# Performance work log

Hardware: AMD Instinct MI355X
Metric: run time of the kernel (lower is better)

## Reference

```python
import math
import jax, jax.numpy as jnp
import numpy as np

B, N, D, H, NI, NL, NS, MID = 32, 2048, 256, 8, 64, 3, 32, 3


def _ln(x, g, b, eps=1e-5):
    m = jnp.mean(x, axis=-1, keepdims=True)
    v = jnp.mean((x - m) ** 2, axis=-1, keepdims=True)
    return (x - m) * jax.lax.rsqrt(v + eps) * g + b


def _mab(Q, K, mask, Wq, bq, Wk, bk, Wv, bv, Wo, bo, g0, b0, g1, b1):
    # torch's split(dim_split,2)+cat(...,0) == reshape to (B, n, H, dh)
    dh = D // H
    q = (Q @ Wq + bq).reshape(Q.shape[0], Q.shape[1], H, dh)
    k = (K @ Wk + bk).reshape(K.shape[0], K.shape[1], H, dh)
    v = (K @ Wv + bv).reshape(K.shape[0], K.shape[1], H, dh)
    A = jnp.einsum('bqhd,bkhd->bhqk', q, k) / math.sqrt(D)  # note: sqrt(dim_V), faithful
    A = jnp.where(mask[:, None, None, :] == 0, -1e4, A)
    A = jax.nn.softmax(A, axis=-1)
    o = q + jnp.einsum('bhqk,bkhd->bqhd', A, v)
    O = o.reshape(Q.shape[0], Q.shape[1], D)
    O = _ln(O, g0, b0)
    O = O + jax.nn.relu(O @ Wo + bo)
    return _ln(O, g1, b1)


def _forward(x_values, y_target, point_mask, proj_W, proj_b, isab_I,
             isab_Wq, isab_bq, isab_Wk, isab_bk, isab_Wv, isab_bv,
             isab_Wo, isab_bo, isab_g0, isab_b0, isab_g1, isab_b1,
             pma_S, pma_Wq, pma_bq, pma_Wk, pma_bk, pma_Wv, pma_bv,
             pma_Wo, pma_bo, pma_g0, pma_b0, pma_g1, pma_b1):
    # input_dim == max_input_dim, so the zero-padded feature build is a concat
    feats = jnp.concatenate([x_values, y_target[..., None]], axis=-1)  # (B, N, MID+1)
    x = jax.nn.gelu(feats @ proj_W + proj_b, approximate=False)
    ones_mask = jnp.ones((x.shape[0], NI), jnp.float32)
    stk = (isab_Wq, isab_bq, isab_Wk, isab_bk, isab_Wv, isab_bv,
           isab_Wo, isab_bo, isab_g0, isab_b0, isab_g1, isab_b1)
    for l in range(NL):
        I = jnp.broadcast_to(isab_I[l][None], (x.shape[0], NI, D))
        h = _mab(I, x, point_mask, *[a[l, 0] for a in stk])   # mab0: inducing pts attend to X
        x = _mab(x, h, ones_mask, *[a[l, 1] for a in stk])    # mab1: X attends to H (all valid)
    S = jnp.broadcast_to(pma_S[None], (x.shape[0], NS, D))
    return _mab(S, x, point_mask, pma_Wq, pma_bq, pma_Wk, pma_bk, pma_Wv,
                pma_bv, pma_Wo, pma_bo, pma_g0, pma_b0, pma_g1, pma_b1)


def setup_inputs():
    key = jax.random.key(0)
    ks = iter(jax.random.split(key, 40))
    def nrm(shape, s=0.05):
        return jax.random.normal(next(ks), shape, dtype=jnp.float32) * s
    z = lambda shape: jnp.zeros(shape, jnp.float32)
    o = lambda shape: jnp.ones(shape, jnp.float32)
    return {
        'x_values': jax.random.normal(next(ks), (B, N, MID), jnp.float32),
        'y_target': jax.random.normal(next(ks), (B, N), jnp.float32),
        'point_mask': jax.random.randint(next(ks), (B, N), 0, 2).astype(jnp.float32),
        'proj_W': nrm((MID + 1, D)), 'proj_b': z((D,)),
        'isab_I': nrm((NL, NI, D), 0.1),
        'isab_Wq': nrm((NL, 2, D, D)), 'isab_bq': z((NL, 2, D)),
        'isab_Wk': nrm((NL, 2, D, D)), 'isab_bk': z((NL, 2, D)),
        'isab_Wv': nrm((NL, 2, D, D)), 'isab_bv': z((NL, 2, D)),
        'isab_Wo': nrm((NL, 2, D, D)), 'isab_bo': z((NL, 2, D)),
        'isab_g0': o((NL, 2, D)), 'isab_b0': z((NL, 2, D)),
        'isab_g1': o((NL, 2, D)), 'isab_b1': z((NL, 2, D)),
        'pma_S': nrm((NS, D), 0.1),
        'pma_Wq': nrm((D, D)), 'pma_bq': z((D,)),
        'pma_Wk': nrm((D, D)), 'pma_bk': z((D,)),
        'pma_Wv': nrm((D, D)), 'pma_bv': z((D,)),
        'pma_Wo': nrm((D, D)), 'pma_bo': z((D,)),
        'pma_g0': o((D,)), 'pma_b0': z((D,)),
        'pma_g1': o((D,)), 'pma_b1': z((D,)),
    }


def reference(x_values, y_target, point_mask, proj_W, proj_b, isab_I,
              isab_Wq, isab_bq, isab_Wk, isab_bk, isab_Wv, isab_bv,
              isab_Wo, isab_bo, isab_g0, isab_b0, isab_g1, isab_b1,
              pma_S, pma_Wq, pma_bq, pma_Wk, pma_bk, pma_Wv, pma_bv,
              pma_Wo, pma_bo, pma_g0, pma_b0, pma_g1, pma_b1):
    return _forward(x_values, y_target, point_mask, proj_W, proj_b, isab_I,
                    isab_Wq, isab_bq, isab_Wk, isab_bk, isab_Wv, isab_bv,
                    isab_Wo, isab_bo, isab_g0, isab_b0, isab_g1, isab_b1,
                    pma_S, pma_Wq, pma_bq, pma_Wk, pma_bk, pma_Wv, pma_bv,
                    pma_Wo, pma_bo, pma_g0, pma_b0, pma_g1, pma_b1)
```

## Files before the change

kernel.cpp:

```cpp
#include <hip/hip_runtime.h>
#include <hip/hip_bf16.h>


typedef __attribute__((ext_vector_type(8))) short short8;
typedef __attribute__((ext_vector_type(4))) float f32x4;
typedef __attribute__((ext_vector_type(4))) ushort ushort4v;

__device__ __forceinline__ ushort f2bf(float f) {
  uint u = __builtin_bit_cast(uint, f);
  u += 0x7fffu + ((u >> 16) & 1u);
  return (ushort)(u >> 16);
}
__device__ __forceinline__ float bf2f(ushort h) {
  uint u = (uint)h << 16;
  return __builtin_bit_cast(float, u);
}

__global__ __launch_bounds__(256) void prep_weights(
    const float* __restrict__ Wq, const float* __restrict__ Wk,
    const float* __restrict__ Wv, const float* __restrict__ Wo,
    const float* __restrict__ pWq, const float* __restrict__ pWk,
    const float* __restrict__ pWv, const float* __restrict__ pWo,
    ushort* __restrict__ wt)
{
  __shared__ float tile[64][65];
  const int m = blockIdx.y;
  const int t = blockIdx.x;
  const int tr = (t >> 2) * 64;
  const int tc = (t & 3) * 64;
  const float* src;
  if (m < 24) {
    int l = m >> 3, s = (m >> 2) & 1, w = m & 3;
    const float* base = (w == 0) ? Wq : (w == 1) ? Wk : (w == 2) ? Wv : Wo;
    src = base + (size_t)(l * 2 + s) * 65536;
  } else {
    int w = m & 3;
    src = (w == 0) ? pWq : (w == 1) ? pWk : (w == 2) ? pWv : pWo;
  }
  const int tid = threadIdx.x;
  const int cn = tid & 63;
  const int rk = tid >> 6;
#pragma unroll
  for (int j = 0; j < 16; ++j) {
    int kl = rk + j * 4;
    tile[kl][cn] = src[(size_t)(tr + kl) * 256 + tc + cn];
  }
  __syncthreads();
  ushort* dst = wt + (size_t)m * 65536;
#pragma unroll
  for (int j = 0; j < 16; ++j) {
    int nl = rk + j * 4;
    dst[(size_t)(tc + nl) * 256 + tr + cn] = f2bf(tile[cn][nl]);
  }
}

__global__ __launch_bounds__(256) void proj_gelu(
    const float* __restrict__ xv, const float* __restrict__ yt,
    const float* __restrict__ pW, const float* __restrict__ pb,
    ushort* __restrict__ xb)
{
  const int d = threadIdx.x;
  const int row0 = blockIdx.x * 8;
  const float w0 = pW[d], w1 = pW[256 + d], w2 = pW[512 + d], w3 = pW[768 + d];
  const float bz = pb[d];
#pragma unroll
  for (int rr = 0; rr < 8; ++rr) {
    int row = row0 + rr;
    float f0 = xv[(size_t)row * 3 + 0];
    float f1 = xv[(size_t)row * 3 + 1];
    float f2 = xv[(size_t)row * 3 + 2];
    float f3 = yt[row];
    float a = bz + f0 * w0 + f1 * w1 + f2 * w2 + f3 * w3;
    float g = 0.5f * a * (1.f + erff(a * 0.70710678118654752f));
    xb[(size_t)row * 256 + d] = f2bf(g);
  }
}

__global__ __launch_bounds__(256) void gemm_q(
    const float* __restrict__ iI, const float* __restrict__ pS,
    const ushort* __restrict__ wt, const float* __restrict__ ibq,
    const float* __restrict__ pbq, ushort* __restrict__ q_all)
{
  const int bq = blockIdx.x;
  const float* A; const ushort* Wt; const float* bias; ushort* out; int M;
  if (bq < 3) { A = iI + bq * 16384; Wt = wt + (size_t)(bq * 8) * 65536; bias = ibq + bq * 512; out = q_all + bq * 16384; M = 64; }
  else        { A = pS; Wt = wt + (size_t)24 * 65536; bias = pbq; out = q_all + 49152; M = 32; }
  const int tid = threadIdx.x;
  const int wave = tid >> 6, lane = tid & 63;
  const int l15 = lane & 15, l4 = lane >> 4, koff = l4 * 8;
  f32x4 acc[4][4];
#pragma unroll
  for (int i = 0; i < 4; ++i)
#pragma unroll
    for (int j = 0; j < 4; ++j) acc[i][j] = (f32x4)0.f;
#pragma unroll
  for (int ks = 0; ks < 8; ++ks) {
    short8 af[4];
#pragma unroll
    for (int mf = 0; mf < 4; ++mf) {
      if (mf * 16 < M) {
        const float* ap = A + (size_t)(mf * 16 + l15) * 256 + ks * 32 + koff;
        float4 f0 = *(const float4*)ap;
        float4 f1 = *(const float4*)(ap + 4);
        short8 sv;
        sv[0] = (short)f2bf(f0.x); sv[1] = (short)f2bf(f0.y);
        sv[2] = (short)f2bf(f0.z); sv[3] = (short)f2bf(f0.w);
        sv[4] = (short)f2bf(f1.x); sv[5] = (short)f2bf(f1.y);
        sv[6] = (short)f2bf(f1.z); sv[7] = (short)f2bf(f1.w);
        af[mf] = sv;
      } else af[mf] = (short8)0;
    }
#pragma unroll
    for (int nf = 0; nf < 4; ++nf) {
      short8 bf = *(const short8*)(Wt + (size_t)(wave * 64 + nf * 16 + l15) * 256 + ks * 32 + koff);
#pragma unroll
      for (int mf = 0; mf < 4; ++mf)
        acc[mf][nf] = __builtin_amdgcn_mfma_f32_16x16x32_bf16(af[mf], bf, acc[mf][nf], 0, 0, 0);
    }
  }
#pragma unroll
  for (int mf = 0; mf < 4; ++mf) {
    if (mf * 16 >= M) continue;
#pragma unroll
    for (int nf = 0; nf < 4; ++nf) {
      int col = wave * 64 + nf * 16 + l15;
      float bcol = bias[col];
#pragma unroll
      for (int r = 0; r < 4; ++r)
        out[(size_t)(mf * 16 + l4 * 4 + r) * 256 + col] = f2bf(acc[mf][nf][r] + bcol);
    }
  }
}

template <int EPI, bool OUTF32, int COLS>
__global__ __launch_bounds__(COLS * 2, (COLS == 128) ? 4 : 2) void gemm_bp(
    const ushort* __restrict__ A,
    const ushort* __restrict__ Wt0, const ushort* __restrict__ Wt1, const ushort* __restrict__ Wt2,
    const float* __restrict__ b0, const float* __restrict__ b1, const float* __restrict__ b2,
    void* __restrict__ o0, void* __restrict__ o1, void* __restrict__ o2,
    const float* __restrict__ lng, const float* __restrict__ lnb,
    int ny, int nyz)
{
  constexpr int WC = COLS / 64;
  constexpr int PS = COLS * 64;
  constexpr int ROWB = COLS * 2;
  __shared__ __align__(16) char Bs[4 * PS];
  __shared__ float redbuf[(EPI == 3) ? 1280 : 4];
  const int bid = blockIdx.x;
  const int bx = bid / nyz;
  const int brem = bid % nyz;
  const int y = brem % ny;
  const int z = brem / ny;
  const ushort* Wt = (z == 0) ? Wt0 : ((z == 1) ? Wt1 : Wt2);
  const float* bias = (z == 0) ? b0 : ((z == 1) ? b1 : b2);
  void* outp = (z == 0) ? o0 : ((z == 1) ? o1 : o2);
  const int pcol = y * COLS;

  const int tid = threadIdx.x;
  const int wave = tid >> 6, lane = tid & 63;
  const int wc = wave % WC, wr = wave / WC;
  const int l15 = lane & 15, l4 = lane >> 4;
  const int row0 = bx * 128;
  const int sn = tid >> 1, sseg = tid & 1;

  f32x4 acc[4][4];
#pragma unroll
  for (int i = 0; i < 4; ++i)
#pragma unroll
    for (int j = 0; j < 4; ++j) acc[i][j] = (f32x4)0.f;

#pragma unroll
  for (int half = 0; half < 2; ++half) {
    if (half) __syncthreads();
    {
      const ushort* src = Wt + (size_t)(pcol + sn) * 256 + half * 128 + sseg * 64;
#pragma unroll
      for (int c = 0; c < 8; ++c) {
        uint4 w = *(const uint4*)(src + c * 8);
        int plane = sseg * 2 + (c >> 2);
        char* dst = Bs + plane * PS + sn * 64 + (((c & 3) * 16) ^ (((sn >> 1) & 3) << 4));
        *(uint4*)dst = w;
      }
    }
    __syncthreads();
#pragma unroll
    for (int ks = 0; ks < 4; ++ks) {
      short8 af[4];
#pragma unroll
      for (int mfa = 0; mfa < 4; ++mfa)
        af[mfa] = *(const short8*)(A + (size_t)(row0 + wr * 64 + mfa * 16 + l15) * 256 + half * 128 + ks * 32 + l4 * 8);
#pragma unroll
      for (int nfb = 0; nfb < 4; ++nfb) {
        int n = wc * 64 + nfb * 16 + l15;
        short8 bf = *(const short8*)(Bs + ks * PS + n * 64 + ((l4 * 16) ^ (((n >> 1) & 3) << 4)));
#pragma unroll
        for (int mfa = 0; mfa < 4; ++mfa)
          acc[mfa][nfb] = __builtin_amdgcn_mfma_f32_16x16x32_bf16(bf, af[mfa], acc[mfa][nfb], 0, 0, 0);
      }
    }
  }

  if constexpr (EPI == 0) {
    __syncthreads();
#pragma unroll
    for (int nfb = 0; nfb < 4; ++nfb) {
      f32x4 bv = *(const f32x4*)(bias + pcol + wc * 64 + nfb * 16 + l4 * 4);
      int colb = wc * 128 + nfb * 32 + l4 * 8;
#pragma unroll
      for (int mfa = 0; mfa < 4; ++mfa) {
        int row = wr * 64 + mfa * 16 + l15;
        ushort4v pk;
#pragma unroll
        for (int i = 0; i < 4; ++i) pk[i] = f2bf(acc[mfa][nfb][i] + bv[i]);
        *(ushort4v*)(Bs + row * ROWB + (colb ^ ((row & 7) << 4))) = pk;
      }
    }
    __syncthreads();
    const int srow = tid >> 2, seg = tid & 3;
#pragma unroll
    for (int rr = 0; rr < 2; ++rr) {
      int row = srow + rr * 64;
      int x = (row & 7) << 4;
      ushort* gdst = (ushort*)outp + (size_t)(row0 + row) * 256 + pcol;
#pragma unroll
      for (int it = 0; it < 4; ++it) {
        int colb = seg * 16 + it * 64;
        uint4 v = *(const uint4*)(Bs + row * ROWB + (colb ^ x));
        *(uint4*)(gdst + colb / 2) = v;
      }
    }
  } else {
    float* red1 = redbuf;
    float* red2 = redbuf + 512;
    float* mv_ = redbuf + 1024;
    float* rv_ = redbuf + 1152;
    float s1[4] = {0.f, 0.f, 0.f, 0.f}, s2[4] = {0.f, 0.f, 0.f, 0.f};
#pragma unroll
    for (int nfb = 0; nfb < 4; ++nfb) {
      int col0 = wc * 64 + nfb * 16 + l4 * 4;
      f32x4 bv = *(const f32x4*)(bias + col0);
#pragma unroll
      for (int mfa = 0; mfa < 4; ++mfa) {
        size_t row = (size_t)row0 + wr * 64 + mfa * 16 + l15;
        ushort4v rz = *(const ushort4v*)(A + row * 256 + col0);
#pragma unroll
        for (int i = 0; i < 4; ++i) {
          float zz = bf2f(rz[i]) + fmaxf(acc[mfa][nfb][i] + bv[i], 0.f);
          acc[mfa][nfb][i] = zz;
          s1[mfa] += zz;
          s2[mfa] += zz * zz;
        }
      }
    }
#pragma unroll
    for (int mfa = 0; mfa < 4; ++mfa) {
      s1[mfa] += __shfl_xor(s1[mfa], 16); s1[mfa] += __shfl_xor(s1[mfa], 32);
      s2[mfa] += __shfl_xor(s2[mfa], 16); s2[mfa] += __shfl_xor(s2[mfa], 32);
    }
    if (l4 == 0) {
#pragma unroll
      for (int mfa = 0; mfa < 4; ++mfa) {
        red1[wc * 128 + wr * 64 + mfa * 16 + l15] = s1[mfa];
        red2[wc * 128 + wr * 64 + mfa * 16 + l15] = s2[mfa];
      }
    }
    __syncthreads();
    if (tid < 128) {
      float m1 = red1[tid] + red1[128 + tid] + red1[256 + tid] + red1[384 + tid];
      float m2 = red2[tid] + red2[128 + tid] + red2[256 + tid] + red2[384 + tid];
      float mean = m1 * 0.00390625f;
      float var = m2 * 0.00390625f - mean * mean;
      mv_[tid] = mean;
      rv_[tid] = rsqrtf(var + 1e-5f);
    }
    __syncthreads();
#pragma unroll
    for (int nfb = 0; nfb < 4; ++nfb) {
      int col0 = wc * 64 + nfb * 16 + l4 * 4;
      f32x4 gg = *(const f32x4*)(lng + col0);
      f32x4 bb = *(const f32x4*)(lnb + col0);
      int colb = col0 * 2;
#pragma unroll
      for (int mfa = 0; mfa < 4; ++mfa) {
        int lr = wr * 64 + mfa * 16 + l15;
        float mean = mv_[lr], rs = rv_[lr];
        if constexpr (OUTF32) {
          f32x4 w;
#pragma unroll
          for (int i = 0; i < 4; ++i) w[i] = (acc[mfa][nfb][i] - mean) * rs * gg[i] + bb[i];
          *(f32x4*)((float*)outp + ((size_t)row0 + lr) * 256 + col0) = w;
        } else {
          ushort4v pk;
#pragma unroll
          for (int i = 0; i < 4; ++i) pk[i] = f2bf((acc[mfa][nfb][i] - mean) * rs * gg[i] + bb[i]);
          *(ushort4v*)(Bs + lr * ROWB + (colb ^ ((lr & 7) << 4))) = pk;
        }
      }
    }
    if constexpr (!OUTF32) {
      __syncthreads();
      const int srow = tid >> 2, seg = tid & 3;
      int x = (srow & 7) << 4;
      ushort* gdst = (ushort*)outp + (size_t)(row0 + srow) * 256;
#pragma unroll
      for (int it = 0; it < 8; ++it) {
        int colb = seg * 16 + it * 64;
        uint4 v = *(const uint4*)(Bs + srow * ROWB + (colb ^ x));
        *(uint4*)(gdst + colb / 2) = v;
      }
    }
  }
}

template <int MF>
__global__ __launch_bounds__(512) void attn_big(
    const ushort* __restrict__ qb, const ushort* __restrict__ kb,
    const ushort* __restrict__ vb, const float* __restrict__ mask,
    ushort* __restrict__ O)
{
  __shared__ __align__(16) ushort Ps[8][64][72];
  __shared__ __align__(16) ushort Vt[8][32][72];
  const int h = blockIdx.x, b = blockIdx.y;
  const int tid = threadIdx.x;
  const int w = tid >> 6, lane = tid & 63;
  const int l15 = lane & 15, l4 = lane >> 4;
  const int koff = l4 * 8;
  const int kvbase = b * 2048;

  short8 qf[MF];
#pragma unroll
  for (int mf = 0; mf < MF; ++mf)
    qf[mf] = *(const short8*)(qb + (size_t)(mf * 16 + l15) * 256 + h * 32 + koff);

  f32x4 Oa[MF][2];
  float Mr[MF][4], Lr[MF][4];
#pragma unroll
  for (int mf = 0; mf < MF; ++mf) {
    Oa[mf][0] = (f32x4)0.f; Oa[mf][1] = (f32x4)0.f;
#pragma unroll
    for (int r = 0; r < 4; ++r) { Mr[mf][r] = -1e30f; Lr[mf][r] = 0.f; }
  }

  for (int c = 0; c < 4; ++c) {
    const int kc = w * 256 + c * 64;
    f32x4 S[MF][4];
#pragma unroll
    for (int nf = 0; nf < 4; ++nf) {
      short8 kf = *(const short8*)(kb + (size_t)(kvbase + kc + nf * 16 + l15) * 256 + h * 32 + koff);
#pragma unroll
      for (int mf = 0; mf < MF; ++mf)
        S[mf][nf] = __builtin_amdgcn_mfma_f32_16x16x32_bf16(qf[mf], kf, (f32x4)0.f, 0, 0, 0);
    }
    float mv[4];
#pragma unroll
    for (int nf = 0; nf < 4; ++nf)
      mv[nf] = mask[(size_t)b * 2048 + kc + nf * 16 + l15];
#pragma unroll
    for (int mf = 0; mf < MF; ++mf)
#pragma unroll
      for (int nf = 0; nf < 4; ++nf)
#pragma unroll
        for (int r = 0; r < 4; ++r) {
          float s = S[mf][nf][r] * 0.0625f;
          S[mf][nf][r] = (mv[nf] != 0.f) ? s : -1e4f;
        }
#pragma unroll
    for (int mf = 0; mf < MF; ++mf)
#pragma unroll
      for (int r = 0; r < 4; ++r) {
        float pm = fmaxf(fmaxf(S[mf][0][r], S[mf][1][r]), fmaxf(S[mf][2][r], S[mf][3][r]));
        pm = fmaxf(pm, __shfl_xor(pm, 1));
        pm = fmaxf(pm, __shfl_xor(pm, 2));
        pm = fmaxf(pm, __shfl_xor(pm, 4));
        pm = fmaxf(pm, __shfl_xor(pm, 8));
        float Mnew = fmaxf(Mr[mf][r], pm);
        float corr = __expf(Mr[mf][r] - Mnew);
        Mr[mf][r] = Mnew;
        float rs = 0.f;
#pragma unroll
        for (int nf = 0; nf < 4; ++nf) {
          float p = __expf(S[mf][nf][r] - Mnew);
          S[mf][nf][r] = p;
          rs += p;
        }
        rs += __shfl_xor(rs, 1);
        rs += __shfl_xor(rs, 2);
        rs += __shfl_xor(rs, 4);
        rs += __shfl_xor(rs, 8);
        Lr[mf][r] = Lr[mf][r] * corr + rs;
        Oa[mf][0][r] *= corr;
        Oa[mf][1][r] *= corr;
      }
#pragma unroll
    for (int dblk = 0; dblk < 4; ++dblk) {
      short8 vv = *(const short8*)(vb + (size_t)(kvbase + kc + lane) * 256 + h * 32 + dblk * 8);
#pragma unroll
      for (int j = 0; j < 8; ++j) Vt[w][dblk * 8 + j][lane] = (ushort)vv[j];
    }
#pragma unroll
    for (int mf = 0; mf < MF; ++mf)
#pragma unroll
      for (int nf = 0; nf < 4; ++nf)
#pragma unroll
        for (int r = 0; r < 4; ++r)
          Ps[w][mf * 16 + l4 * 4 + r][nf * 16 + l15] = f2bf(S[mf][nf][r]);
#pragma unroll
    for (int ks = 0; ks < 2; ++ks) {
      short8 pf[MF];
#pragma unroll
      for (int mf = 0; mf < MF; ++mf)
        pf[mf] = *(const short8*)&Ps[w][mf * 16 + l15][ks * 32 + koff];
#pragma unroll
      for (int nf2 = 0; nf2 < 2; ++nf2) {
        short8 vf = *(const short8*)&Vt[w][nf2 * 16 + l15][ks * 32 + koff];
#pragma unroll
        for (int mf = 0; mf < MF; ++mf)
          Oa[mf][nf2] = __builtin_amdgcn_mfma_f32_16x16x32_bf16(pf[mf], vf, Oa[mf][nf2], 0, 0, 0);
      }
    }
  }

  __syncthreads();
  float* Mw = (float*)&Ps[0][0][0];
  float* Lw = Mw + 512;
  float* Ow = Lw + 512;
#pragma unroll
  for (int mf = 0; mf < MF; ++mf)
#pragma unroll
    for (int r = 0; r < 4; ++r) {
      int row = mf * 16 + l4 * 4 + r;
      if (l15 == 0) { Mw[w * 64 + row] = Mr[mf][r]; Lw[w * 64 + row] = Lr[mf][r]; }
#pragma unroll
      for (int nf2 = 0; nf2 < 2; ++nf2)
        Ow[(w * 64 + row) * 33 + nf2 * 16 + l15] = Oa[mf][nf2][r];
    }
  __syncthreads();
  const int NQ = MF * 16;
  int row = tid >> 3, dg = tid & 7;
  if (row < NQ) {
    float mm = -1e30f;
#pragma unroll
    for (int s = 0; s < 8; ++s) mm = fmaxf(mm, Mw[s * 64 + row]);
    float den = 0.f, es[8];
#pragma unroll
    for (int s = 0; s < 8; ++s) {
      es[s] = __expf(Mw[s * 64 + row] - mm);
      den += Lw[s * 64 + row] * es[s];
    }
    float invden = 1.f / den;
    ushort4v pk;
#pragma unroll
    for (int i = 0; i < 4; ++i) {
      int d = dg * 4 + i;
      float num = 0.f;
#pragma unroll
      for (int s = 0; s < 8; ++s) num += Ow[(s * 64 + row) * 33 + d] * es[s];
      float qv = bf2f(qb[(size_t)row * 256 + h * 32 + d]);
      pk[i] = f2bf(qv + num * invden);
    }
    *(ushort4v*)(O + (size_t)(b * NQ + row) * 256 + h * 32 + dg * 4) = pk;
  }
}

__global__ __launch_bounds__(512) void attn_small(
    const ushort* __restrict__ qb, const ushort* __restrict__ kb,
    const ushort* __restrict__ vb, const float* __restrict__ lng,
    const float* __restrict__ lnb, ushort* __restrict__ O)
{
  __shared__ __align__(16) ushort Ps[8][64][72];
  __shared__ __align__(16) ushort Vt[8][32][72];
  __shared__ float red1[8][64], red2[8][64], mv_[64], rv_[64];
  const int qt = blockIdx.x, b = blockIdx.y;
  const int tid = threadIdx.x;
  const int w = tid >> 6, lane = tid & 63;
  const int l15 = lane & 15, l4 = lane >> 4;
  const int koff = l4 * 8;
  const size_t qrow0 = (size_t)b * 2048 + qt * 64;
  const int kvbase = b * 64;
  const int h = w;

  short8 qf[4];
#pragma unroll
  for (int mf = 0; mf < 4; ++mf)
    qf[mf] = *(const short8*)(qb + (qrow0 + mf * 16 + l15) * 256 + h * 32 + koff);

  f32x4 S[4][4];
#pragma unroll
  for (int nf = 0; nf < 4; ++nf) {
    short8 kf = *(const short8*)(kb + (size_t)(kvbase + nf * 16 + l15) * 256 + h * 32 + koff);
#pragma unroll
    for (int mf = 0; mf < 4; ++mf)
      S[mf][nf] = __builtin_amdgcn_mfma_f32_16x16x32_bf16(qf[mf], kf, (f32x4)0.f, 0, 0, 0);
  }
  float Lr[4][4];
#pragma unroll
  for (int mf = 0; mf < 4; ++mf)
#pragma unroll
    for (int r = 0; r < 4; ++r) {
      float pm = fmaxf(fmaxf(S[mf][0][r], S[mf][1][r]), fmaxf(S[mf][2][r], S[mf][3][r])) * 0.0625f;
      pm = fmaxf(pm, __shfl_xor(pm, 1));
      pm = fmaxf(pm, __shfl_xor(pm, 2));
      pm = fmaxf(pm, __shfl_xor(pm, 4));
      pm = fmaxf(pm, __shfl_xor(pm, 8));
      float rs = 0.f;
#pragma unroll
      for (int nf = 0; nf < 4; ++nf) {
        float p = __expf(S[mf][nf][r] * 0.0625f - pm);
        S[mf][nf][r] = p;
        rs += p;
      }
      rs += __shfl_xor(rs, 1);
      rs += __shfl_xor(rs, 2);
      rs += __shfl_xor(rs, 4);
      rs += __shfl_xor(rs, 8);
      Lr[mf][r] = rs;
    }
#pragma unroll
  for (int dblk = 0; dblk < 4; ++dblk) {
    short8 vv = *(const short8*)(vb + (size_t)(kvbase + lane) * 256 + h * 32 + dblk * 8);
#pragma unroll
    for (int j = 0; j < 8; ++j) Vt[w][dblk * 8 + j][lane] = (ushort)vv[j];
  }
#pragma unroll
  for (int mf = 0; mf < 4; ++mf)
#pragma unroll
    for (int nf = 0; nf < 4; ++nf)
#pragma unroll
      for (int r = 0; r < 4; ++r)
        Ps[w][mf * 16 + l4 * 4 + r][nf * 16 + l15] = f2bf(S[mf][nf][r]);
  f32x4 Oa[4][2];
#pragma unroll
  for (int mf = 0; mf < 4; ++mf) { Oa[mf][0] = (f32x4)0.f; Oa[mf][1] = (f32x4)0.f; }
#pragma unroll
  for (int ks = 0; ks < 2; ++ks) {
    short8 pf[4];
#pragma unroll
    for (int mf = 0; mf < 4; ++mf)
      pf[mf] = *(const short8*)&Ps[w][mf * 16 + l15][ks * 32 + koff];
#pragma unroll
    for (int nf2 = 0; nf2 < 2; ++nf2) {
      short8 vf = *(const short8*)&Vt[w][nf2 * 16 + l15][ks * 32 + koff];
#pragma unroll
      for (int mf = 0; mf < 4; ++mf)
        Oa[mf][nf2] = __builtin_amdgcn_mfma_f32_16x16x32_bf16(pf[mf], vf, Oa[mf][nf2], 0, 0, 0);
    }
  }
  float s1[4][4], s2[4][4];
#pragma unroll
  for (int mf = 0; mf < 4; ++mf)
#pragma unroll
    for (int r = 0; r < 4; ++r) {
      float invL = 1.f / Lr[mf][r];
      s1[mf][r] = 0.f; s2[mf][r] = 0.f;
#pragma unroll
      for (int nf2 = 0; nf2 < 2; ++nf2) {
        int col = h * 32 + nf2 * 16 + l15;
        size_t row = qrow0 + mf * 16 + l4 * 4 + r;
        float z = bf2f(qb[row * 256 + col]) + Oa[mf][nf2][r] * invL;
        Oa[mf][nf2][r] = z;
        s1[mf][r] += z;
        s2[mf][r] += z * z;
      }
#pragma unroll
      for (int off = 1; off < 16; off <<= 1) {
        s1[mf][r] += __shfl_xor(s1[mf][r], off);
        s2[mf][r] += __shfl_xor(s2[mf][r], off);
      }
      if (l15 == 0) {
        int row = mf * 16 + l4 * 4 + r;
        red1[w][row] = s1[mf][r];
        red2[w][row] = s2[mf][r];
      }
    }
  __syncthreads();
  if (tid < 64) {
    float m1 = 0.f, m2 = 0.f;
#pragma unroll
    for (int s = 0; s < 8; ++s) { m1 += red1[s][tid]; m2 += red2[s][tid]; }
    float mean = m1 * 0.00390625f;
    float var = m2 * 0.00390625f - mean * mean;
    mv_[tid] = mean;
    rv_[tid] = rsqrtf(var + 1e-5f);
  }
  __syncthreads();
#pragma unroll
  for (int nf2 = 0; nf2 < 2; ++nf2) {
    int col = h * 32 + nf2 * 16 + l15;
    float gc = lng[col], bc = lnb[col];
#pragma unroll
    for (int mf = 0; mf < 4; ++mf)
#pragma unroll
      for (int r = 0; r < 4; ++r) {
        int row = mf * 16 + l4 * 4 + r;
        float v = (Oa[mf][nf2][r] - mv_[row]) * rv_[row] * gc + bc;
        O[(qrow0 + row) * 256 + col] = f2bf(v);
      }
  }
}

__global__ __launch_bounds__(256) void ln4(
    const ushort* __restrict__ in, ushort* __restrict__ out,
    const float* __restrict__ g, const float* __restrict__ bb)
{
  const int w = threadIdx.x >> 6, lane = threadIdx.x & 63;
  const size_t row = (size_t)blockIdx.x * 4 + w;
  ushort4v u = *(const ushort4v*)(in + row * 256 + lane * 4);
  float v[4];
#pragma unroll
  for (int i = 0; i < 4; ++i) v[i] = bf2f(u[i]);
  float s1 = v[0] + v[1] + v[2] + v[3];
  float s2 = v[0] * v[0] + v[1] * v[1] + v[2] * v[2] + v[3] * v[3];
#pragma unroll
  for (int off = 1; off < 64; off <<= 1) {
    s1 += __shfl_xor(s1, off);
    s2 += __shfl_xor(s2, off);
  }
  float mean = s1 * 0.00390625f;
  float var = s2 * 0.00390625f - mean * mean;
  float rs = rsqrtf(var + 1e-5f);
  f32x4 gg = *(const f32x4*)(g + lane * 4);
  f32x4 bv = *(const f32x4*)(bb + lane * 4);
  ushort4v p;
#pragma unroll
  for (int i = 0; i < 4; ++i) p[i] = f2bf((v[i] - mean) * rs * gg[i] + bv[i]);
  *(ushort4v*)(out + row * 256 + lane * 4) = p;
}

extern "C" void kernel_launch(void* const* d_in, const int* in_sizes, int n_in,
                              void* d_out, int out_size, void* d_ws, size_t ws_size,
                              hipStream_t stream) {
  const float* xv = (const float*)d_in[0];
  const float* yt = (const float*)d_in[1];
  const float* pmask = (const float*)d_in[2];
  const float* prW = (const float*)d_in[3];
  const float* prb = (const float*)d_in[4];
  const float* iI = (const float*)d_in[5];
  const float* iWq = (const float*)d_in[6];
  const float* ibq = (const float*)d_in[7];
  const float* iWk = (const float*)d_in[8];
  const float* ibk = (const float*)d_in[9];
  const float* iWv = (const float*)d_in[10];
  const float* ibv = (const float*)d_in[11];
  const float* iWo = (const float*)d_in[12];
  const float* ibo = (const float*)d_in[13];
  const float* ig0 = (const float*)d_in[14];
  const float* ib0 = (const float*)d_in[15];
  const float* ig1 = (const float*)d_in[16];
  const float* ib1 = (const float*)d_in[17];
  const float* pS = (const float*)d_in[18];
  const float* pWq = (const float*)d_in[19];
  const float* pbq = (const float*)d_in[20];
  const float* pWk = (const float*)d_in[21];
  const float* pbk = (const float*)d_in[22];
  const float* pWv = (const float*)d_in[23];
  const float* pbv = (const float*)d_in[24];
  const float* pWo = (const float*)d_in[25];
  const float* pbo = (const float*)d_in[26];
  const float* pg0 = (const float*)d_in[27];
  const float* pb0 = (const float*)d_in[28];
  const float* pg1 = (const float*)d_in[29];
  const float* pb1 = (const float*)d_in[30];

  char* ws = (char*)d_ws;
  if (ws_size < 172621824u) return;
  ushort* xb = (ushort*)(ws + 0);
  ushort* ob = (ushort*)(ws + 33554432);
  ushort* hb = (ushort*)(ws + 67108864);
  ushort* qbw = (ushort*)(ws + 68157440);
  ushort* kbw = (ushort*)(ws + 101711872);
  ushort* vbw = (ushort*)(ws + 135266304);
  ushort* wt = (ushort*)(ws + 168820736);
  ushort* q_all = (ushort*)(ws + 172490752);

  prep_weights<<<dim3(16, 28), 256, 0, stream>>>(iWq, iWk, iWv, iWo, pWq, pWk, pWv, pWo, wt);
  proj_gelu<<<8192, 256, 0, stream>>>(xv, yt, prW, prb, xb);
  gemm_q<<<4, 256, 0, stream>>>(iI, pS, wt, ibq, pbq, q_all);

  for (int l = 0; l < 3; ++l) {
    const int s0 = l * 2, s1 = l * 2 + 1;
    const ushort* wk = wt + (size_t)(l * 8 + 1) * 65536;
    const ushort* wv = wt + (size_t)(l * 8 + 2) * 65536;
    const ushort* wo0 = wt + (size_t)(l * 8 + 3) * 65536;
    const ushort* wq1 = wt + (size_t)(l * 8 + 4) * 65536;
    const ushort* wk1 = wt + (size_t)(l * 8 + 5) * 65536;
    const ushort* wv1 = wt + (size_t)(l * 8 + 6) * 65536;
    const ushort* wo1 = wt + (size_t)(l * 8 + 7) * 65536;
    gemm_bp<0, false, 128><<<3072, 256, 0, stream>>>(
        xb, wk, wv, wq1, ibk + s0 * 256, ibv + s0 * 256, ibq + s1 * 256,
        kbw, vbw, qbw, nullptr, nullptr, 2, 6);
    attn_big<4><<<dim3(8, 32), 512, 0, stream>>>(q_all + l * 16384, kbw, vbw, pmask, ob);
    ln4<<<512, 256, 0, stream>>>(ob, ob, ig0 + s0 * 256, ib0 + s0 * 256);
    gemm_bp<3, false, 256><<<16, 512, 0, stream>>>(
        ob, wo0, wo0, wo0, ibo + s0 * 256, ibo + s0 * 256, ibo + s0 * 256,
        hb, hb, hb, ig1 + s0 * 256, ib1 + s0 * 256, 1, 1);
    gemm_bp<0, false, 128><<<64, 256, 0, stream>>>(
        hb, wk1, wv1, wv1, ibk + s1 * 256, ibv + s1 * 256, ibv + s1 * 256,
        kbw, vbw, vbw, nullptr, nullptr, 2, 4);
    attn_small<<<dim3(32, 32), 512, 0, stream>>>(qbw, kbw, vbw, ig0 + s1 * 256, ib0 + s1 * 256, ob);
    gemm_bp<3, false, 256><<<512, 512, 0, stream>>>(
        ob, wo1, wo1, wo1, ibo + s1 * 256, ibo + s1 * 256, ibo + s1 * 256,
        xb, xb, xb, ig1 + s1 * 256, ib1 + s1 * 256, 1, 1);
  }
  gemm_bp<0, false, 128><<<2048, 256, 0, stream>>>(
      xb, wt + (size_t)25 * 65536, wt + (size_t)26 * 65536, wt + (size_t)26 * 65536,
      pbk, pbv, pbv, kbw, vbw, vbw, nullptr, nullptr, 2, 4);
  attn_big<2><<<dim3(8, 32), 512, 0, stream>>>(q_all + 49152, kbw, vbw, pmask, ob);
  ln4<<<256, 256, 0, stream>>>(ob, ob, pg0, pb0);
  gemm_bp<3, true, 256><<<8, 512, 0, stream>>>(
      ob, wt + (size_t)27 * 65536, wt + (size_t)27 * 65536, wt + (size_t)27 * 65536,
      pbo, pbo, pbo, d_out, d_out, d_out, pg1, pb1, 1, 1);
}
```

Before: 872.4 us.

## Loop over output matrices inside each GEMM block to reuse A-tile reads

The batched projection GEMM no longer gives each block a separate 128-column slice of one output matrix. Each 512-thread block now covers all 256 columns and loops over the NZ weight matrices (K/V/Q) inside the kernel. This cuts grid size and lets the block's 128 input rows stay cache-resident across the fused projections. The staging buffer uses row padding instead of an XOR swizzle for the epilogue. Costs are fewer blocks (less parallelism for the small GEMMs), higher register pressure under launch_bounds(512,4), and serialized matrices within a block.

```diff
diff --git a/kernel.cpp b/kernel.cpp
--- a/kernel.cpp
+++ b/kernel.cpp
@@ -132,181 +132,170 @@
   }
 }
 
-template <int EPI, bool OUTF32, int COLS>
-__global__ __launch_bounds__(COLS * 2, (COLS == 128) ? 4 : 2) void gemm_bp(
+template <int EPI, bool OUTF32, int NZ>
+__global__ __launch_bounds__(512, 4) void gemm_bp(
     const ushort* __restrict__ A,
     const ushort* __restrict__ Wt0, const ushort* __restrict__ Wt1, const ushort* __restrict__ Wt2,
     const float* __restrict__ b0, const float* __restrict__ b1, const float* __restrict__ b2,
     void* __restrict__ o0, void* __restrict__ o1, void* __restrict__ o2,
-    const float* __restrict__ lng, const float* __restrict__ lnb,
-    int ny, int nyz)
+    const float* __restrict__ lng, const float* __restrict__ lnb)
 {
-  constexpr int WC = COLS / 64;
-  constexpr int PS = COLS * 64;
-  constexpr int ROWB = COLS * 2;
-  __shared__ __align__(16) char Bs[4 * PS];
+  constexpr int PS = 256 * 64;
+  constexpr int ROWB = 512 + 16;
+  __shared__ __align__(16) char Bs[128 * ROWB];
   __shared__ float redbuf[(EPI == 3) ? 1280 : 4];
-  const int bid = blockIdx.x;
-  const int bx = bid / nyz;
-  const int brem = bid % nyz;
-  const int y = brem % ny;
-  const int z = brem / ny;
-  const ushort* Wt = (z == 0) ? Wt0 : ((z == 1) ? Wt1 : Wt2);
-  const float* bias = (z == 0) ? b0 : ((z == 1) ? b1 : b2);
-  void* outp = (z == 0) ? o0 : ((z == 1) ? o1 : o2);
-  const int pcol = y * COLS;
 
   const int tid = threadIdx.x;
   const int wave = tid >> 6, lane = tid & 63;
-  const int wc = wave % WC, wr = wave / WC;
+  const int wc = wave & 3, wr = wave >> 2;
   const int l15 = lane & 15, l4 = lane >> 4;
-  const int row0 = bx * 128;
+  const int row0 = blockIdx.x * 128;
   const int sn = tid >> 1, sseg = tid & 1;
 
-  f32x4 acc[4][4];
-#pragma unroll
-  for (int i = 0; i < 4; ++i)
-#pragma unroll
-    for (int j = 0; j < 4; ++j) acc[i][j] = (f32x4)0.f;
-
-#pragma unroll
-  for (int half = 0; half < 2; ++half) {
-    if (half) __syncthreads();
-    {
-      const ushort* src = Wt + (size_t)(pcol + sn) * 256 + half * 128 + sseg * 64;
-#pragma unroll
-      for (int c = 0; c < 8; ++c) {
-        uint4 w = *(const uint4*)(src + c * 8);
-        int plane = sseg * 2 + (c >> 2);
-        char* dst = Bs + plane * PS + sn * 64 + (((c & 3) * 16) ^ (((sn >> 1) & 3) << 4));
-        *(uint4*)dst = w;
-      }
-    }
-    __syncthreads();
-#pragma unroll
-    for (int ks = 0; ks < 4; ++ks) {
-      short8 af[4];
-#pragma unroll
-      for (int mfa = 0; mfa < 4; ++mfa)
-        af[mfa] = *(const short8*)(A + (size_t)(row0 + wr * 64 + mfa * 16 + l15) * 256 + half * 128 + ks * 32 + l4 * 8);
+#pragma unroll
+  for (int z = 0; z < NZ; ++z) {
+    const ushort* Wt = (z == 0) ? Wt0 : ((z == 1) ? Wt1 : Wt2);
+    const float* bias = (z == 0) ? b0 : ((z == 1) ? b1 : b2);
+    void* outp = (z == 0) ? o0 : ((z == 1) ? o1 : o2);
+
+    f32x4 acc[4][4];
+#pragma unroll
+    for (int i = 0; i < 4; ++i)
+#pragma unroll
+      for (int j = 0; j < 4; ++j) acc[i][j] = (f32x4)0.f;
+
+#pragma unroll
+    for (int half = 0; half < 2; ++half) {
+      if (z || half) __syncthreads();
+      {
+        const ushort* src = Wt + (size_t)sn * 256 + half * 128 + sseg * 64;
+#pragma unroll
+        for (int c = 0; c < 8; ++c) {
+          uint4 w = *(const uint4*)(src + c * 8);
+          int plane = sseg * 2 + (c >> 2);
+          char* dst = Bs + plane * PS + sn * 64 + (((c & 3) * 16) ^ (((sn >> 1) & 3) << 4));
+          *(uint4*)dst = w;
+        }
+      }
+      __syncthreads();
+#pragma unroll
+      for (int ks = 0; ks < 4; ++ks) {
+        short8 af[4];
+#pragma unroll
+        for (int mfa = 0; mfa < 4; ++mfa)
+          af[mfa] = *(const short8*)(A + (size_t)(row0 + wr * 64 + mfa * 16 + l15) * 256 + half * 128 + ks * 32 + l4 * 8);
+#pragma unroll
+        for (int nfb = 0; nfb < 4; ++nfb) {
+          int n = wc * 64 + nfb * 16 + l15;
+          short8 bf = *(const short8*)(Bs + ks * PS + n * 64 + ((l4 * 16) ^ (((n >> 1) & 3) << 4)));
+#pragma unroll
+          for (int mfa = 0; mfa < 4; ++mfa)
+            acc[mfa][nfb] = __builtin_amdgcn_mfma_f32_16x16x32_bf16(bf, af[mfa], acc[mfa][nfb], 0, 0, 0);
+        }
+      }
+    }
+
+    if constexpr (EPI == 0) {
+      __syncthreads();
 #pragma unroll
       for (int nfb = 0; nfb < 4; ++nfb) {
-        int n = wc * 64 + nfb * 16 + l15;
-        short8 bf = *(const short8*)(Bs + ks * PS + n * 64 + ((l4 * 16) ^ (((n >> 1) & 3) << 4)));
-#pragma unroll
-        for (int mfa = 0; mfa < 4; ++mfa)
-          acc[mfa][nfb] = __builtin_amdgcn_mfma_f32_16x16x32_bf16(bf, af[mfa], acc[mfa][nfb], 0, 0, 0);
-      }
-    }
-  }
-
-  if constexpr (EPI == 0) {
-    __syncthreads();
-#pragma unroll
-    for (int nfb = 0; nfb < 4; ++nfb) {
-      f32x4 bv = *(const f32x4*)(bias + pcol + wc * 64 + nfb * 16 + l4 * 4);
-      int colb = wc * 128 + nfb * 32 + l4 * 8;
-#pragma unroll
-      for (int mfa = 0; mfa < 4; ++mfa) {
-        int row = wr * 64 + mfa * 16 + l15;
-        ushort4v pk;
-#pragma unroll
-        for (int i = 0; i < 4; ++i) pk[i] = f2bf(acc[mfa][nfb][i] + bv[i]);
-        *(ushort4v*)(Bs + row * ROWB + (colb ^ ((row & 7) << 4))) = pk;
-      }
-    }
-    __syncthreads();
-    const int srow = tid >> 2, seg = tid & 3;
-#pragma unroll
-    for (int rr = 0; rr < 2; ++rr) {
-      int row = srow + rr * 64;
-      int x = (row & 7) << 4;
-      ushort* gdst = (ushort*)outp + (size_t)(row0 + row) * 256 + pcol;
-#pragma unroll
-      for (int it = 0; it < 4; ++it) {
-        int colb = seg * 16 + it * 64;
-        uint4 v = *(const uint4*)(Bs + row * ROWB + (colb ^ x));
-        *(uint4*)(gdst + colb / 2) = v;
-      }
-    }
-  } else {
-    float* red1 = redbuf;
-    float* red2 = redbuf + 512;
-    float* mv_ = redbuf + 1024;
-    float* rv_ = redbuf + 1152;
-    float s1[4] = {0.f, 0.f, 0.f, 0.f}, s2[4] = {0.f, 0.f, 0.f, 0.f};
-#pragma unroll
-    for (int nfb = 0; nfb < 4; ++nfb) {
-      int col0 = wc * 64 + nfb * 16 + l4 * 4;
-      f32x4 bv = *(const f32x4*)(bias + col0);
-#pragma unroll
-      for (int mfa = 0; mfa < 4; ++mfa) {
-        size_t row = (size_t)row0 + wr * 64 + mfa * 16 + l15;
-        ushort4v rz = *(const ushort4v*)(A + row * 256 + col0);
-#pragma unroll
-        for (int i = 0; i < 4; ++i) {
-          float zz = bf2f(rz[i]) + fmaxf(acc[mfa][nfb][i] + bv[i], 0.f);
-          acc[mfa][nfb][i] = zz;
-          s1[mfa] += zz;
-          s2[mfa] += zz * zz;
-        }
-      }
-    }
-#pragma unroll
-    for (int mfa = 0; mfa < 4; ++mfa) {
-      s1[mfa] += __shfl_xor(s1[mfa], 16); s1[mfa] += __shfl_xor(s1[mfa], 32);
-      s2[mfa] += __shfl_xor(s2[mfa], 16); s2[mfa] += __shfl_xor(s2[mfa], 32);
-    }
-    if (l4 == 0) {
-#pragma unroll
-      for (int mfa = 0; mfa < 4; ++mfa) {
-        red1[wc * 128 + wr * 64 + mfa * 16 + l15] = s1[mfa];
-        red2[wc * 128 + wr * 64 + mfa * 16 + l15] = s2[mfa];
-      }
-    }
-    __syncthreads();
-    if (tid < 128) {
-      float m1 = red1[tid] + red1[128 + tid] + red1[256 + tid] + red1[384 + tid];
-      float m2 = red2[tid] + red2[128 + tid] + red2[256 + tid] + red2[384 + tid];
-      float mean = m1 * 0.00390625f;
-      float var = m2 * 0.00390625f - mean * mean;
-      mv_[tid] = mean;
-      rv_[tid] = rsqrtf(var + 1e-5f);
-    }
-    __syncthreads();
-#pragma unroll
-    for (int nfb = 0; nfb < 4; ++nfb) {
-      int col0 = wc * 64 + nfb * 16 + l4 * 4;
-      f32x4 gg = *(const f32x4*)(lng + col0);
-      f32x4 bb = *(const f32x4*)(lnb + col0);
-      int colb = col0 * 2;
-#pragma unroll
-      for (int mfa = 0; mfa < 4; ++mfa) {
-        int lr = wr * 64 + mfa * 16 + l15;
-        float mean = mv_[lr], rs = rv_[lr];
-        if constexpr (OUTF32) {
-          f32x4 w;
-#pragma unroll
-          for (int i = 0; i < 4; ++i) w[i] = (acc[mfa][nfb][i] - mean) * rs * gg[i] + bb[i];
-          *(f32x4*)((float*)outp + ((size_t)row0 + lr) * 256 + col0) = w;
-        } else {
+        int col0 = wc * 64 + nfb * 16 + l4 * 4;
+        f32x4 bv = *(const f32x4*)(bias + col0);
+#pragma unroll
+        for (int mfa = 0; mfa < 4; ++mfa) {
+          int row = wr * 64 + mfa * 16 + l15;
           ushort4v pk;
 #pragma unroll
-          for (int i = 0; i < 4; ++i) pk[i] = f2bf((acc[mfa][nfb][i] - mean) * rs * gg[i] + bb[i]);
-          *(ushort4v*)(Bs + lr * ROWB + (colb ^ ((lr & 7) << 4))) = pk;
-        }
-      }
-    }
-    if constexpr (!OUTF32) {
+          for (int i = 0; i < 4; ++i) pk[i] = f2bf(acc[mfa][nfb][i] + bv[i]);
+          *(ushort4v*)(Bs + row * ROWB + col0 * 2) = pk;
+        }
+      }
       __syncthreads();
       const int srow = tid >> 2, seg = tid & 3;
-      int x = (srow & 7) << 4;
       ushort* gdst = (ushort*)outp + (size_t)(row0 + srow) * 256;
 #pragma unroll
       for (int it = 0; it < 8; ++it) {
         int colb = seg * 16 + it * 64;
-        uint4 v = *(const uint4*)(Bs + srow * ROWB + (colb ^ x));
+        uint4 v = *(const uint4*)(Bs + srow * ROWB + colb);
         *(uint4*)(gdst + colb / 2) = v;
+      }
+    } else {
+      float* red1 = redbuf;
+      float* red2 = redbuf + 512;
+      float* mv_ = redbuf + 1024;
+      float* rv_ = redbuf + 1152;
+      float s1[4] = {0.f, 0.f, 0.f, 0.f}, s2[4] = {0.f, 0.f, 0.f, 0.f};
+#pragma unroll
+      for (int nfb = 0; nfb < 4; ++nfb) {
+        int col0 = wc * 64 + nfb * 16 + l4 * 4;
+        f32x4 bv = *(const f32x4*)(bias + col0);
+#pragma unroll
+        for (int mfa = 0; mfa < 4; ++mfa) {
+          size_t row = (size_t)row0 + wr * 64 + mfa * 16 + l15;
+          ushort4v rz = *(const ushort4v*)(A + row * 256 + col0);
+#pragma unroll
+          for (int i = 0; i < 4; ++i) {
+            float zz = bf2f(rz[i]) + fmaxf(acc[mfa][nfb][i] + bv[i], 0.f);
+            acc[mfa][nfb][i] = zz;
+            s1[mfa] += zz;
+            s2[mfa] += zz * zz;
+          }
+        }
+      }
+#pragma unroll
+      for (int mfa = 0; mfa < 4; ++mfa) {
+        s1[mfa] += __shfl_xor(s1[mfa], 16); s1[mfa] += __shfl_xor(s1[mfa], 32);
+        s2[mfa] += __shfl_xor(s2[mfa], 16); s2[mfa] += __shfl_xor(s2[mfa], 32);
+      }
+      if (l4 == 0) {
+#pragma unroll
+        for (int mfa = 0; mfa < 4; ++mfa) {
+          red1[wc * 128 + wr * 64 + mfa * 16 + l15] = s1[mfa];
+          red2[wc * 128 + wr * 64 + mfa * 16 + l15] = s2[mfa];
+        }
+      }
+      __syncthreads();
+      if (tid < 128) {
+        float m1 = red1[tid] + red1[128 + tid] + red1[256 + tid] + red1[384 + tid];
+        float m2 = red2[tid] + red2[128 + tid] + red2[256 + tid] + red2[384 + tid];
+        float mean = m1 * 0.00390625f;
+        float var = m2 * 0.00390625f - mean * mean;
+        mv_[tid] = mean;
+        rv_[tid] = rsqrtf(var + 1e-5f);
+      }
+      __syncthreads();
+#pragma unroll
+      for (int nfb = 0; nfb < 4; ++nfb) {
+        int col0 = wc * 64 + nfb * 16 + l4 * 4;
+        f32x4 gg = *(const f32x4*)(lng + col0);
+        f32x4 bb = *(const f32x4*)(lnb + col0);
+#pragma unroll
+        for (int mfa = 0; mfa < 4; ++mfa) {
+          int lr = wr * 64 + mfa * 16 + l15;
+          float mean = mv_[lr], rs = rv_[lr];
+          if constexpr (OUTF32) {
+            f32x4 w;
+#pragma unroll
+            for (int i = 0; i < 4; ++i) w[i] = (acc[mfa][nfb][i] - mean) * rs * gg[i] + bb[i];
+            *(f32x4*)((float*)outp + ((size_t)row0 + lr) * 256 + col0) = w;
+          } else {
+            ushort4v pk;
+#pragma unroll
+            for (int i = 0; i < 4; ++i) pk[i] = f2bf((acc[mfa][nfb][i] - mean) * rs * gg[i] + bb[i]);
+            *(ushort4v*)(Bs + lr * ROWB + col0 * 2) = pk;
+          }
+        }
+      }
+      if constexpr (!OUTF32) {
+        __syncthreads();
+        const int srow = tid >> 2, seg = tid & 3;
+        ushort* gdst = (ushort*)outp + (size_t)(row0 + srow) * 256;
+#pragma unroll
+        for (int it = 0; it < 8; ++it) {
+          int colb = seg * 16 + it * 64;
+          uint4 v = *(const uint4*)(Bs + srow * ROWB + colb);
+          *(uint4*)(gdst + colb / 2) = v;
+        }
       }
     }
   }
@@ -685,28 +674,28 @@
     const ushort* wk1 = wt + (size_t)(l * 8 + 5) * 65536;
     const ushort* wv1 = wt + (size_t)(l * 8 + 6) * 65536;
     const ushort* wo1 = wt + (size_t)(l * 8 + 7) * 65536;
-    gemm_bp<0, false, 128><<<3072, 256, 0, stream>>>(
+    gemm_bp<0, false, 3><<<512, 512, 0, stream>>>(
         xb, wk, wv, wq1, ibk + s0 * 256, ibv + s0 * 256, ibq + s1 * 256,
-        kbw, vbw, qbw, nullptr, nullptr, 2, 6);
+        kbw, vbw, qbw, nullptr, nullptr);
     attn_big<4><<<dim3(8, 32), 512, 0, stream>>>(q_all + l * 16384, kbw, vbw, pmask, ob);
     ln4<<<512, 256, 0, stream>>>(ob, ob, ig0 + s0 * 256, ib0 + s0 * 256);
-    gemm_bp<3, false, 256><<<16, 512, 0, stream>>>(
+    gemm_bp<3, false, 1><<<16, 512, 0, stream>>>(
         ob, wo0, wo0, wo0, ibo + s0 * 256, ibo + s0 * 256, ibo + s0 * 256,
-        hb, hb, hb, ig1 + s0 * 256, ib1 + s0 * 256, 1, 1);
-    gemm_bp<0, false, 128><<<64, 256, 0, stream>>>(
+        hb, hb, hb, ig1 + s0 * 256, ib1 + s0 * 256);
+    gemm_bp<0, false, 2><<<16, 512, 0, stream>>>(
         hb, wk1, wv1, wv1, ibk + s1 * 256, ibv + s1 * 256, ibv + s1 * 256,
-        kbw, vbw, vbw, nullptr, nullptr, 2, 4);
+        kbw, vbw, vbw, nullptr, nullptr);
     attn_small<<<dim3(32, 32), 512, 0, stream>>>(qbw, kbw, vbw, ig0 + s1 * 256, ib0 + s1 * 256, ob);
-    gemm_bp<3, false, 256><<<512, 512, 0, stream>>>(
+    gemm_bp<3, false, 1><<<512, 512, 0, stream>>>(
         ob, wo1, wo1, wo1, ibo + s1 * 256, ibo + s1 * 256, ibo + s1 * 256,
-        xb, xb, xb, ig1 + s1 * 256, ib1 + s1 * 256, 1, 1);
-  }
-  gemm_bp<0, false, 128><<<2048, 256, 0, stream>>>(
+        xb, xb, xb, ig1 + s1 * 256, ib1 + s1 * 256);
+  }
+  gemm_bp<0, false, 2><<<512, 512, 0, stream>>>(
       xb, wt + (size_t)25 * 65536, wt + (size_t)26 * 65536, wt + (size_t)26 * 65536,
-      pbk, pbv, pbv, kbw, vbw, vbw, nullptr, nullptr, 2, 4);
+      pbk, pbv, pbv, kbw, vbw, vbw, nullptr, nullptr);
   attn_big<2><<<dim3(8, 32), 512, 0, stream>>>(q_all + 49152, kbw, vbw, pmask, ob);
   ln4<<<256, 256, 0, stream>>>(ob, ob, pg0, pb0);
-  gemm_bp<3, true, 256><<<8, 512, 0, stream>>>(
+  gemm_bp<3, true, 1><<<8, 512, 0, stream>>>(
       ob, wt + (size_t)27 * 65536, wt + (size_t)27 * 65536, wt + (size_t)27 * 65536,
-      pbo, pbo, pbo, d_out, d_out, d_out, pg1, pb1, 1, 1);
-}
+      pbo, pbo, pbo, d_out, d_out, d_out, pg1, pb1);
+}
```

New measurement: 948.3 us. 8.7% more time.

## Fuse mab1 Q projection, attention, LN, output projection and LN into one kernel

Applied to the files above, without the earlier changes.

The mab1 Q projection is moved out of the batched K/V/Q GEMM into the attention kernel, which also now performs the Wo projection, ReLU residual and the second LayerNorm in shared memory. Each block computes Q for its 64 rows and stores it in LDS. It then runs attention and LN0, runs the output GEMM from LDS, and writes the final x back in place. This removes the global round trips of the Q buffer and the intermediate attention output, plus one kernel launch per layer. The cost is higher LDS use, occupancy limited to one block per CU, and weight tiles reread per block from global/L2 with no LDS staging.

```diff
diff --git a/kernel.cpp b/kernel.cpp
--- a/kernel.cpp
+++ b/kernel.cpp
@@ -462,27 +462,67 @@
   }
 }
 
-__global__ __launch_bounds__(512) void attn_small(
-    const ushort* __restrict__ qb, const ushort* __restrict__ kb,
-    const ushort* __restrict__ vb, const float* __restrict__ lng,
-    const float* __restrict__ lnb, ushort* __restrict__ O)
+__global__ __launch_bounds__(512, 1) void mab1_fused(
+    const ushort* __restrict__ xb, const ushort* __restrict__ wq,
+    const float* __restrict__ bq,
+    const ushort* __restrict__ kb, const ushort* __restrict__ vb,
+    const ushort* __restrict__ wo, const float* __restrict__ bo,
+    const float* __restrict__ g0, const float* __restrict__ b0v,
+    const float* __restrict__ g1, const float* __restrict__ b1v,
+    ushort* __restrict__ outb)
 {
+  __shared__ __align__(16) ushort Qs[8][64][40];
   __shared__ __align__(16) ushort Ps[8][64][72];
   __shared__ __align__(16) ushort Vt[8][32][72];
   __shared__ float red1[8][64], red2[8][64], mv_[64], rv_[64];
+  ushort* o_s = &Ps[0][0][0];
+  constexpr int OS = 264;
+
   const int qt = blockIdx.x, b = blockIdx.y;
   const int tid = threadIdx.x;
   const int w = tid >> 6, lane = tid & 63;
   const int l15 = lane & 15, l4 = lane >> 4;
   const int koff = l4 * 8;
-  const size_t qrow0 = (size_t)b * 2048 + qt * 64;
+  const size_t row0 = (size_t)b * 2048 + qt * 64;
   const int kvbase = b * 64;
   const int h = w;
 
+  {
+    f32x4 qa[4][2];
+#pragma unroll
+    for (int i = 0; i < 4; ++i) { qa[i][0] = (f32x4)0.f; qa[i][1] = (f32x4)0.f; }
+#pragma unroll
+    for (int ks = 0; ks < 8; ++ks) {
+      short8 af[4];
+#pragma unroll
+      for (int mfa = 0; mfa < 4; ++mfa)
+        af[mfa] = *(const short8*)(xb + (row0 + mfa * 16 + l15) * 256 + ks * 32 + koff);
+#pragma unroll
+      for (int nfb = 0; nfb < 2; ++nfb) {
+        int n = w * 32 + nfb * 16 + l15;
+        short8 bf = *(const short8*)(wq + (size_t)n * 256 + ks * 32 + koff);
+#pragma unroll
+        for (int mfa = 0; mfa < 4; ++mfa)
+          qa[mfa][nfb] = __builtin_amdgcn_mfma_f32_16x16x32_bf16(bf, af[mfa], qa[mfa][nfb], 0, 0, 0);
+      }
+    }
+#pragma unroll
+    for (int nfb = 0; nfb < 2; ++nfb) {
+      f32x4 bv = *(const f32x4*)(bq + w * 32 + nfb * 16 + l4 * 4);
+#pragma unroll
+      for (int mfa = 0; mfa < 4; ++mfa) {
+        ushort4v pk;
+#pragma unroll
+        for (int i = 0; i < 4; ++i) pk[i] = f2bf(qa[mfa][nfb][i] + bv[i]);
+        *(ushort4v*)&Qs[w][mfa * 16 + l15][nfb * 16 + l4 * 4] = pk;
+      }
+    }
+  }
+
   short8 qf[4];
 #pragma unroll
   for (int mf = 0; mf < 4; ++mf)
-    qf[mf] = *(const short8*)(qb + (qrow0 + mf * 16 + l15) * 256 + h * 32 + koff);
+    qf[mf] = *(const short8*)&Qs[w][mf * 16 + l15][koff];
 
   f32x4 S[4][4];
 #pragma unroll
@@ -545,33 +585,35 @@
         Oa[mf][nf2] = __builtin_amdgcn_mfma_f32_16x16x32_bf16(pf[mf], vf, Oa[mf][nf2], 0, 0, 0);
     }
   }
-  float s1[4][4], s2[4][4];
-#pragma unroll
-  for (int mf = 0; mf < 4; ++mf)
-#pragma unroll
-    for (int r = 0; r < 4; ++r) {
-      float invL = 1.f / Lr[mf][r];
-      s1[mf][r] = 0.f; s2[mf][r] = 0.f;
-#pragma unroll
-      for (int nf2 = 0; nf2 < 2; ++nf2) {
-        int col = h * 32 + nf2 * 16 + l15;
-        size_t row = qrow0 + mf * 16 + l4 * 4 + r;
-        float z = bf2f(qb[row * 256 + col]) + Oa[mf][nf2][r] * invL;
-        Oa[mf][nf2][r] = z;
-        s1[mf][r] += z;
-        s2[mf][r] += z * z;
-      }
-#pragma unroll
-      for (int off = 1; off < 16; off <<= 1) {
-        s1[mf][r] += __shfl_xor(s1[mf][r], off);
-        s2[mf][r] += __shfl_xor(s2[mf][r], off);
-      }
-      if (l15 == 0) {
-        int row = mf * 16 + l4 * 4 + r;
-        red1[w][row] = s1[mf][r];
-        red2[w][row] = s2[mf][r];
-      }
-    }
+
+  {
+    float s1[4][4], s2[4][4];
+#pragma unroll
+    for (int mf = 0; mf < 4; ++mf)
+#pragma unroll
+      for (int r = 0; r < 4; ++r) {
+        float invL = 1.f / Lr[mf][r];
+        s1[mf][r] = 0.f; s2[mf][r] = 0.f;
+#pragma unroll
+        for (int nf2 = 0; nf2 < 2; ++nf2) {
+          float qv = bf2f(Qs[w][mf * 16 + l4 * 4 + r][nf2 * 16 + l15]);
+          float z = qv + Oa[mf][nf2][r] * invL;
+          Oa[mf][nf2][r] = z;
+          s1[mf][r] += z;
+          s2[mf][r] += z * z;
+        }
+#pragma unroll
+        for (int off = 1; off < 16; off <<= 1) {
+          s1[mf][r] += __shfl_xor(s1[mf][r], off);
+          s2[mf][r] += __shfl_xor(s2[mf][r], off);
+        }
+        if (l15 == 0) {
+          int row = mf * 16 + l4 * 4 + r;
+          red1[w][row] = s1[mf][r];
+          red2[w][row] = s2[mf][r];
+        }
+      }
+  }
   __syncthreads();
   if (tid < 64) {
     float m1 = 0.f, m2 = 0.f;
@@ -586,15 +628,102 @@
 #pragma unroll
   for (int nf2 = 0; nf2 < 2; ++nf2) {
     int col = h * 32 + nf2 * 16 + l15;
-    float gc = lng[col], bc = lnb[col];
+    float gc = g0[col], bc = b0v[col];
 #pragma unroll
     for (int mf = 0; mf < 4; ++mf)
 #pragma unroll
       for (int r = 0; r < 4; ++r) {
         int row = mf * 16 + l4 * 4 + r;
         float v = (Oa[mf][nf2][r] - mv_[row]) * rv_[row] * gc + bc;
-        O[(qrow0 + row) * 256 + col] = f2bf(v);
-      }
+        o_s[row * OS + col] = f2bf(v);
+      }
+  }
+  __syncthreads();
+
+  f32x4 oa[4][2];
+#pragma unroll
+  for (int i = 0; i < 4; ++i) { oa[i][0] = (f32x4)0.f; oa[i][1] = (f32x4)0.f; }
+#pragma unroll
+  for (int ks = 0; ks < 8; ++ks) {
+    short8 af[4];
+#pragma unroll
+    for (int mfa = 0; mfa < 4; ++mfa)
+      af[mfa] = *(const short8*)&o_s[(mfa * 16 + l15) * OS + ks * 32 + koff];
+#pragma unroll
+    for (int nfb = 0; nfb < 2; ++nfb) {
+      int n = w * 32 + nfb * 16 + l15;
+      short8 bf = *(const short8*)(wo + (size_t)n * 256 + ks * 32 + koff);
+#pragma unroll
+      for (int mfa = 0; mfa < 4; ++mfa)
+        oa[mfa][nfb] = __builtin_amdgcn_mfma_f32_16x16x32_bf16(bf, af[mfa], oa[mfa][nfb], 0, 0, 0);
+    }
+  }
+  float t1[4] = {0.f, 0.f, 0.f, 0.f}, t2[4] = {0.f, 0.f, 0.f, 0.f};
+#pragma unroll
+  for (int nfb = 0; nfb < 2; ++nfb) {
+    int col0 = w * 32 + nfb * 16 + l4 * 4;
+    f32x4 bv = *(const f32x4*)(bo + col0);
+#pragma unroll
+    for (int mfa = 0; mfa < 4; ++mfa) {
+      int row = mfa * 16 + l15;
+      ushort4v rz = *(const ushort4v*)&o_s[row * OS + col0];
+#pragma unroll
+      for (int i = 0; i < 4; ++i) {
+        float zz = bf2f(rz[i]) + fmaxf(oa[mfa][nfb][i] + bv[i], 0.f);
+        oa[mfa][nfb][i] = zz;
+        t1[mfa] += zz;
+        t2[mfa] += zz * zz;
+      }
+    }
+  }
+#pragma unroll
+  for (int mfa = 0; mfa < 4; ++mfa) {
+    t1[mfa] += __shfl_xor(t1[mfa], 16); t1[mfa] += __shfl_xor(t1[mfa], 32);
+    t2[mfa] += __shfl_xor(t2[mfa], 16); t2[mfa] += __shfl_xor(t2[mfa], 32);
+  }
+  if (l4 == 0) {
+#pragma unroll
+    for (int mfa = 0; mfa < 4; ++mfa) {
+      red1[w][mfa * 16 + l15] = t1[mfa];
+      red2[w][mfa * 16 + l15] = t2[mfa];
+    }
+  }
+  __syncthreads();
+  if (tid < 64) {
+    float m1 = 0.f, m2 = 0.f;
+#pragma unroll
+    for (int s = 0; s < 8; ++s) { m1 += red1[s][tid]; m2 += red2[s][tid]; }
+    float mean = m1 * 0.00390625f;
+    float var = m2 * 0.00390625f - mean * mean;
+    mv_[tid] = mean;
+    rv_[tid] = rsqrtf(var + 1e-5f);
+  }
+  __syncthreads();
+#pragma unroll
+  for (int nfb = 0; nfb < 2; ++nfb) {
+    int col0 = w * 32 + nfb * 16 + l4 * 4;
+    f32x4 gg = *(const f32x4*)(g1 + col0);
+    f32x4 bb = *(const f32x4*)(b1v + col0);
+#pragma unroll
+    for (int mfa = 0; mfa < 4; ++mfa) {
+      int row = mfa * 16 + l15;
+      ushort4v pk;
+#pragma unroll
+      for (int i = 0; i < 4; ++i)
+        pk[i] = f2bf((oa[mfa][nfb][i] - mv_[row]) * rv_[row] * gg[i] + bb[i]);
+      *(ushort4v*)&o_s[row * OS + col0] = pk;
+    }
+  }
+  __syncthreads();
+  {
+    const int r_ = tid >> 3, sg = tid & 7;
+    ushort* gdst = outb + (row0 + r_) * 256 + sg * 32;
+    const ushort* src = &o_s[r_ * OS + sg * 32];
+#pragma unroll
+    for (int it = 0; it < 4; ++it) {
+      uint4 v = *(const uint4*)(src + it * 8);
+      *(uint4*)(gdst + it * 8) = v;
+    }
   }
 }
 
@@ -666,7 +795,6 @@
   ushort* xb = (ushort*)(ws + 0);
   ushort* ob = (ushort*)(ws + 33554432);
   ushort* hb = (ushort*)(ws + 67108864);
-  ushort* qbw = (ushort*)(ws + 68157440);
   ushort* kbw = (ushort*)(ws + 101711872);
   ushort* vbw = (ushort*)(ws + 135266304);
   ushort* wt = (ushort*)(ws + 168820736);
@@ -685,9 +813,9 @@
     const ushort* wk1 = wt + (size_t)(l * 8 + 5) * 65536;
     const ushort* wv1 = wt + (size_t)(l * 8 + 6) * 65536;
     const ushort* wo1 = wt + (size_t)(l * 8 + 7) * 65536;
-    gemm_bp<0, false, 128><<<3072, 256, 0, stream>>>(
-        xb, wk, wv, wq1, ibk + s0 * 256, ibv + s0 * 256, ibq + s1 * 256,
-        kbw, vbw, qbw, nullptr, nullptr, 2, 6);
+    gemm_bp<0, false, 128><<<2048, 256, 0, stream>>>(
+        xb, wk, wv, wv, ibk + s0 * 256, ibv + s0 * 256, ibv + s0 * 256,
+        kbw, vbw, vbw, nullptr, nullptr, 2, 4);
     attn_big<4><<<dim3(8, 32), 512, 0, stream>>>(q_all + l * 16384, kbw, vbw, pmask, ob);
     ln4<<<512, 256, 0, stream>>>(ob, ob, ig0 + s0 * 256, ib0 + s0 * 256);
     gemm_bp<3, false, 256><<<16, 512, 0, stream>>>(
@@ -696,10 +824,9 @@
     gemm_bp<0, false, 128><<<64, 256, 0, stream>>>(
         hb, wk1, wv1, wv1, ibk + s1 * 256, ibv + s1 * 256, ibv + s1 * 256,
         kbw, vbw, vbw, nullptr, nullptr, 2, 4);
-    attn_small<<<dim3(32, 32), 512, 0, stream>>>(qbw, kbw, vbw, ig0 + s1 * 256, ib0 + s1 * 256, ob);
-    gemm_bp<3, false, 256><<<512, 512, 0, stream>>>(
-        ob, wo1, wo1, wo1, ibo + s1 * 256, ibo + s1 * 256, ibo + s1 * 256,
-        xb, xb, xb, ig1 + s1 * 256, ib1 + s1 * 256, 1, 1);
+    mab1_fused<<<dim3(32, 32), 512, 0, stream>>>(
+        xb, wq1, ibq + s1 * 256, kbw, vbw, wo1, ibo + s1 * 256,
+        ig0 + s1 * 256, ib0 + s1 * 256, ig1 + s1 * 256, ib1 + s1 * 256, xb);
   }
   gemm_bp<0, false, 128><<<2048, 256, 0, stream>>>(
       xb, wt + (size_t)25 * 65536, wt + (size_t)26 * 65536, wt + (size_t)26 * 65536,
```

New measurement: 866.7 us. No clear change (-0.7%).
